# Kernel optimization log

Hardware: AMD Instinct MI355X
Metric: run time of the kernel (lower is better)

## Reference

```python
import jax, jax.numpy as jnp
import numpy as np

DN = ('NCHW', 'OIHW', 'NCHW')  # dimension numbers for all convs


def _dwconv(x, w, dim):
    # depthwise conv, valid padding; w: (dim,1,kh,kw)
    return jax.lax.conv_general_dilated(
        x, w, window_strides=(1, 1), padding='VALID',
        dimension_numbers=DN, feature_group_count=dim)


def setup_inputs() -> dict:
    key = jax.random.key(0)
    ks = jax.random.split(key, 5)
    B, C, H, W = 16, 256, 96, 96
    REP_K = 3
    x = jax.random.normal(ks[0], (B, C, H, W), dtype=jnp.float32)
    meta_pe = jax.random.normal(ks[1], (1, C, H, 1), dtype=jnp.float32) * 0.02
    weight = jax.random.normal(ks[2], (C, 1, H, 1), dtype=jnp.float32) * 0.02
    bias = jnp.zeros((C,), dtype=jnp.float32)
    rep_weight = jax.random.normal(ks[3], (C, 1, REP_K, 1), dtype=jnp.float32) * 0.02
    return {'x': x, 'meta_pe': meta_pe, 'weight': weight, 'bias': bias,
            'rep_weight': rep_weight}


def reference(x, meta_pe, weight, bias, rep_weight):
    # type == 'H': circular padding / conv along the H axis (kernels (K,1))
    dim = x.shape[1]
    rep_k = rep_weight.shape[2]
    # positional embedding add (broadcast over batch and W)
    x = x + meta_pe
    # local branch: circular pad by rep_k-1 rows, small depthwise conv
    x_cat = jnp.concatenate([x, x[:, :, :rep_k - 1, :]], axis=2)
    x_rep = _dwconv(x_cat, rep_weight, dim)
    # global branch: circular pad by H-1 rows, full-height depthwise conv + bias
    x_cat = jnp.concatenate([x, x[:, :, :-1, :]], axis=2)
    x_gcc = _dwconv(x_cat, weight, dim) + bias[None, :, None, None]
    return x_rep + x_gcc
```

## Files before the change

### kernel.cpp

```cpp
#include <hip/hip_runtime.h>

#define B_    16
#define C_    256
#define HH    96
#define WW    96
#define W4    24
#define TYN   8
#define HPT   12
#define TPB   (W4 * TYN)

__global__ __launch_bounds__(TPB, 3) void fused_circ_conv(
    const float* __restrict__ x,
    const float* __restrict__ meta_pe,
    const float* __restrict__ weight,
    const float* __restrict__ bias,
    const float* __restrict__ rep_weight,
    float* __restrict__ out)
{
    __shared__ float sX[HH * WW];
    __shared__ float sWext[2 * HH];

    const int tid = threadIdx.x;
    const int blk = blockIdx.x;
    const int c = blk & (C_ - 1);

    const size_t base = (size_t)blk * (HH * WW);
    const float4* __restrict__ xg4 = (const float4*)(x + base);

    {
        int k = (tid < HH) ? tid : (tid - HH);
        float wv = weight[c * HH + k];
        if (k < 3) wv += rep_weight[c * 3 + k];
        sWext[tid] = wv;
    }

    {
        float4* sX4 = (float4*)sX;
        const float* mp = meta_pe + c * HH;
#pragma unroll
        for (int r = 0; r < 12; ++r) {
            int i = tid + TPB * r;
            float4 v = xg4[i];
            float m = mp[i / W4];
            v.x += m; v.y += m; v.z += m; v.w += m;
            sX4[i] = v;
        }
    }
    __syncthreads();

    const int tx = tid % W4;
    const int ty = tid / W4;
    const int h0 = ty * HPT;

    float4 acc[HPT];
#pragma unroll
    for (int i = 0; i < HPT; ++i) acc[i] = make_float4(0.f, 0.f, 0.f, 0.f);

    float win[12];
#pragma unroll
    for (int t = 1; t < 12; ++t) win[t] = sWext[84 + t - h0];

    const float4* __restrict__ xrow = (const float4*)sX + tx;
    const float* __restrict__ wrow = sWext + (96 - h0);

    for (int jj = 0; jj < 96; jj += 12) {
#pragma unroll
        for (int r = 0; r < 12; ++r) {
            const int j = jj + r;
            win[r] = wrow[j];
            float4 xv = xrow[j * W4];
#pragma unroll
            for (int i = 0; i < HPT; ++i) {
                float wv = win[(r - i + 12) % 12];
                acc[i].x += wv * xv.x;
                acc[i].y += wv * xv.y;
                acc[i].z += wv * xv.z;
                acc[i].w += wv * xv.w;
            }
        }
    }

    const float bv = bias[c];
    float4* og4 = (float4*)(out + base);
#pragma unroll
    for (int i = 0; i < HPT; ++i) {
        float4 v = acc[i];
        v.x += bv; v.y += bv; v.z += bv; v.w += bv;
        og4[(h0 + i) * W4 + tx] = v;
    }
}

extern "C" void kernel_launch(void* const* d_in, const int* in_sizes, int n_in,
                              void* d_out, int out_size, void* d_ws, size_t ws_size,
                              hipStream_t stream) {
    const float* x          = (const float*)d_in[0];
    const float* meta_pe    = (const float*)d_in[1];
    const float* weight     = (const float*)d_in[2];
    const float* bias       = (const float*)d_in[3];
    const float* rep_weight = (const float*)d_in[4];
    float* out = (float*)d_out;

    fused_circ_conv<<<dim3(B_ * C_), dim3(TPB), 0, stream>>>(
        x, meta_pe, weight, bias, rep_weight, out);
}
```

Baseline: 273.8 us.

## Split each channel plane into two width halves with smaller per-thread row tiles

Each block now handles half the width (48 columns) of a (b,c) plane, so shared memory per block halves and the grid doubles. Each thread computes 6 output rows instead of 12, which cuts accumulator registers, and launch bounds are raised to allow 6 blocks per CU. The aim is higher occupancy and better latency hiding. In exchange, every thread does less register-level reuse of each loaded x value per weight window, and the weight setup and staging work per block is repeated for each half.

```diff
diff --git a/kernel.cpp b/kernel.cpp
--- a/kernel.cpp
+++ b/kernel.cpp
@@ -4,12 +4,13 @@
 #define C_    256
 #define HH    96
 #define WW    96
-#define W4    24
-#define TYN   8
-#define HPT   12
-#define TPB   (W4 * TYN)
+#define WT    48
+#define WT4   (WT / 4)
+#define TYN   16
+#define HPT   6
+#define TPB   (WT4 * TYN)
 
-__global__ __launch_bounds__(TPB, 3) void fused_circ_conv(
+__global__ __launch_bounds__(TPB, 6) void fused_circ_conv(
     const float* __restrict__ x,
     const float* __restrict__ meta_pe,
     const float* __restrict__ weight,
@@ -17,14 +18,15 @@
     const float* __restrict__ rep_weight,
     float* __restrict__ out)
 {
-    __shared__ float sX[HH * WW];
+    __shared__ float sX[HH * WT];
     __shared__ float sWext[2 * HH];
 
     const int tid = threadIdx.x;
-    const int blk = blockIdx.x;
-    const int c = blk & (C_ - 1);
+    const int bc = blockIdx.x >> 1;
+    const int wh = blockIdx.x & 1;
+    const int c = bc & (C_ - 1);
 
-    const size_t base = (size_t)blk * (HH * WW);
+    const size_t base = (size_t)bc * (HH * WW);
     const float4* __restrict__ xg4 = (const float4*)(x + base);
 
     {
@@ -38,40 +40,42 @@
         float4* sX4 = (float4*)sX;
         const float* mp = meta_pe + c * HH;
 #pragma unroll
-        for (int r = 0; r < 12; ++r) {
+        for (int r = 0; r < 6; ++r) {
             int i = tid + TPB * r;
-            float4 v = xg4[i];
-            float m = mp[i / W4];
+            int row = i / WT4;
+            int col = i - row * WT4;
+            float4 v = xg4[row * (WW / 4) + wh * WT4 + col];
+            float m = mp[row];
             v.x += m; v.y += m; v.z += m; v.w += m;
             sX4[i] = v;
         }
     }
     __syncthreads();
 
-    const int tx = tid % W4;
-    const int ty = tid / W4;
+    const int tx = tid % WT4;
+    const int ty = tid / WT4;
     const int h0 = ty * HPT;
 
     float4 acc[HPT];
 #pragma unroll
     for (int i = 0; i < HPT; ++i) acc[i] = make_float4(0.f, 0.f, 0.f, 0.f);
 
-    float win[12];
+    float win[HPT];
 #pragma unroll
-    for (int t = 1; t < 12; ++t) win[t] = sWext[84 + t - h0];
+    for (int t = 1; t < HPT; ++t) win[t] = sWext[90 + t - h0];
 
     const float4* __restrict__ xrow = (const float4*)sX + tx;
     const float* __restrict__ wrow = sWext + (96 - h0);
 
-    for (int jj = 0; jj < 96; jj += 12) {
+    for (int jj = 0; jj < HH; jj += HPT) {
 #pragma unroll
-        for (int r = 0; r < 12; ++r) {
+        for (int r = 0; r < HPT; ++r) {
             const int j = jj + r;
             win[r] = wrow[j];
-            float4 xv = xrow[j * W4];
+            float4 xv = xrow[j * WT4];
 #pragma unroll
             for (int i = 0; i < HPT; ++i) {
-                float wv = win[(r - i + 12) % 12];
+                float wv = win[(r - i + HPT) % HPT];
                 acc[i].x += wv * xv.x;
                 acc[i].y += wv * xv.y;
                 acc[i].z += wv * xv.z;
@@ -86,7 +90,7 @@
     for (int i = 0; i < HPT; ++i) {
         float4 v = acc[i];
         v.x += bv; v.y += bv; v.z += bv; v.w += bv;
-        og4[(h0 + i) * W4 + tx] = v;
+        og4[(h0 + i) * (WW / 4) + wh * WT4 + tx] = v;
     }
 }
 
@@ -100,6 +104,6 @@
     const float* rep_weight = (const float*)d_in[4];
     float* out = (float*)d_out;
 
-    fused_circ_conv<<<dim3(B_ * C_), dim3(TPB), 0, stream>>>(
+    fused_circ_conv<<<dim3(B_ * C_ * 2), dim3(TPB), 0, stream>>>(
         x, meta_pe, weight, bias, rep_weight, out);
 }
```

Measured after the change: 280.7 us. +2.5%, slower.
